# Kernel tuning notes

Measured on AMD Instinct MI355X. Metric: run time of the kernel, lower is better.

The kernel has to match this reference:

```python
import jax, jax.numpy as jnp
import numpy as np

DEPTH, FEAT, HID = 20, 2048, 1024
HALF = FEAT // 2
CLAMP = 2.0
TWO_OVER_PI = 0.6366197723675814  # FrEIA's 0.636619772


def setup_inputs() -> dict:
    key = jax.random.key(0)
    ks = jax.random.split(key, 9)
    x = jax.random.normal(ks[0], (4096, FEAT), dtype=jnp.float32)
    # FrEIA PermuteRandom: numpy permutation seeded with layer index k
    perms = jnp.asarray(
        np.stack([np.random.RandomState(k).permutation(FEAT) for k in range(DEPTH)]),
        dtype=jnp.int32,
    )
    def w(k, shape):  # module reinits all params as 0.01*randn
        return 0.01 * jax.random.normal(k, shape, dtype=jnp.float32)
    return {
        "x": x, "perms": perms,
        "s1_w1": w(ks[1], (DEPTH, HALF, HID)), "s1_b1": w(ks[2], (DEPTH, HID)),
        "s1_w2": w(ks[3], (DEPTH, HID, FEAT)), "s1_b2": w(ks[4], (DEPTH, FEAT)),
        "s2_w1": w(ks[5], (DEPTH, HALF, HID)), "s2_b1": w(ks[6], (DEPTH, HID)),
        "s2_w2": w(ks[7], (DEPTH, HID, FEAT)), "s2_b2": w(ks[8], (DEPTH, FEAT)),
    }


def _subnet(x, w1, b1, w2, b2):
    h = x @ w1 + b1
    h = jnp.where(h >= 0, h, 0.01 * h)  # LeakyReLU(negative_slope=0.01)
    return h @ w2 + b2


def reference(x, perms, s1_w1, s1_b1, s1_w2, s1_b2, s2_w1, s2_b1, s2_w2, s2_b2):
    def body(carry, xs):
        z, jac = carry
        perm, w1a, b1a, w1b, b1b, w2a, b2a, w2b, b2b = xs
        z = z[:, perm]                       # PermuteRandom
        x1, x2 = z[:, :HALF], z[:, HALF:]    # GLOW coupling split
        r2 = _subnet(x2, w2a, b2a, w2b, b2b)  # [B, FEAT] -> (s2, t2)
        e2 = CLAMP * TWO_OVER_PI * jnp.arctan(r2[:, :HALF] / CLAMP)
        y1 = jnp.exp(e2) * x1 + r2[:, HALF:]
        r1 = _subnet(y1, w1a, b1a, w1b, b1b)  # (s1, t1)
        e1 = CLAMP * TWO_OVER_PI * jnp.arctan(r1[:, :HALF] / CLAMP)
        y2 = jnp.exp(e1) * x2 + r1[:, HALF:]
        jac = jac + e1.sum(-1) + e2.sum(-1)  # log|det J| per sample
        return (jnp.concatenate([y1, y2], axis=-1), jac), None

    jac0 = jnp.zeros(x.shape[0], dtype=x.dtype)
    (z, jac), _ = jax.lax.scan(
        body, (x, jac0),
        (perms, s1_w1, s1_b1, s1_w2, s1_b2, s2_w1, s2_b1, s2_w2, s2_b2),
    )
    return z, jac
```

## Files before the change

kernel.cpp:

```cpp
#include <hip/hip_runtime.h>
#include <stdint.h>

#define DEPTH 20
#define FEAT  2048
#define HALF  1024
#define HID   1024
#define MROWS 4096

typedef __bf16 bf16x8 __attribute__((ext_vector_type(8)));
typedef float  f32x4  __attribute__((ext_vector_type(4)));
typedef unsigned int u32x4 __attribute__((ext_vector_type(4)));

__device__ __forceinline__ unsigned short f2bf(float f) {
  union { float f; unsigned int u; } v; v.f = f;
  unsigned int u = v.u + 0x7fffu + ((v.u >> 16) & 1u);
  return (unsigned short)(u >> 16);
}

__device__ __forceinline__ void async_cp16(unsigned short* lds, const unsigned short* g) {
  __builtin_amdgcn_global_load_lds(
      (const __attribute__((address_space(1))) void*)g,
      (__attribute__((address_space(3))) void*)lds, 16, 0, 0);
}

__device__ __forceinline__ bf16x8 lds_ld8(const unsigned short* p) {
  return __builtin_bit_cast(bf16x8, *(const u32x4*)p);
}

__global__ void wcvt_k(const float* __restrict__ s2w1, const float* __restrict__ s2w2,
                       const float* __restrict__ s1w1, const float* __restrict__ s1w2,
                       unsigned short* __restrict__ w2a, unsigned short* __restrict__ w2b,
                       unsigned short* __restrict__ w1a, unsigned short* __restrict__ w1b) {
  const int zid = blockIdx.z;
  const int d = zid >> 2, which = zid & 3;
  const float* src; unsigned short* dst; int N, pp;
  switch (which) {
    case 0:  src = s2w1 + (size_t)d * HALF * HID;  dst = w2a + (size_t)d * HALF * HID; N = 1024; pp = 0; break;
    case 1:  src = s2w2 + (size_t)d * HID * FEAT;  dst = w2b + (size_t)d * FEAT * HID; N = 2048; pp = 1; break;
    case 2:  src = s1w1 + (size_t)d * HALF * HID;  dst = w1a + (size_t)d * HALF * HID; N = 1024; pp = 0; break;
    default: src = s1w2 + (size_t)d * HID * FEAT;  dst = w1b + (size_t)d * FEAT * HID; N = 2048; pp = 1; break;
  }
  int nb = blockIdx.x * 32;
  if (nb >= N) return;
  int kb = blockIdx.y * 32;
  __shared__ float t[32][33];
  int tx = threadIdx.x, ty = threadIdx.y;
#pragma unroll
  for (int s = 0; s < 4; ++s)
    t[ty + 8*s][tx] = src[(size_t)(kb + ty + 8*s) * N + nb + tx];
  __syncthreads();
  int pbase = pp ? (nb < 1024 ? 2*nb : 2*(nb - 1024) + 32) : nb;
#pragma unroll
  for (int s = 0; s < 4; ++s) {
    int nl = ty + 8*s;
    dst[(size_t)(pbase + nl) * 1024 + kb + tx] = f2bf(t[tx][nl]);
  }
}

__device__ __forceinline__ int porig(int p) {
  int g = p >> 6, o = p & 63;
  return (o < 32) ? (g*32 + o) : (1024 + g*32 + (o - 32));
}

__global__ void bias_k(const float* __restrict__ s2b1, const float* __restrict__ s2b2,
                       const float* __restrict__ s1b1, const float* __restrict__ s1b2,
                       float* __restrict__ b2a, float* __restrict__ b2b,
                       float* __restrict__ b1a, float* __restrict__ b1b) {
  int i = blockIdx.x * 256 + threadIdx.x;
  if (i >= DEPTH * 6144) return;
  int d = i / 6144, j = i - d * 6144;
  if (j < 1024)      b2a[d*1024 + j] = s2b1[(size_t)d*HID + j];
  else if (j < 3072) { int p = j - 1024; b2b[d*2048 + p] = s2b2[(size_t)d*FEAT + porig(p)]; }
  else if (j < 4096) b1a[d*1024 + j - 3072] = s1b1[(size_t)d*HID + j - 3072];
  else               { int p = j - 4096; b1b[d*2048 + p] = s1b2[(size_t)d*FEAT + porig(p)]; }
}

__global__ void permute_k(const float* __restrict__ z, const int* __restrict__ perm,
                          float* __restrict__ x1f, float* __restrict__ x2f,
                          unsigned short* __restrict__ x2b) {
  int c = blockIdx.x * 256 + threadIdx.x;
  int row0 = blockIdx.y * 8;
  int pc = perm[c];
#pragma unroll
  for (int r = 0; r < 8; ++r) {
    int row = row0 + r;
    float v = z[row * FEAT + pc];
    if (c < HALF) {
      x1f[row * HALF + c] = v;
    } else {
      x2f[row * HALF + c - HALF] = v;
      x2b[row * HALF + c - HALF] = f2bf(v);
    }
  }
}

template<int EPI>
__launch_bounds__(256)
__global__ void gemm_k(const unsigned short* __restrict__ A,
                       const unsigned short* __restrict__ Bt,
                       const float* __restrict__ bias,
                       const float* __restrict__ xin,
                       float* __restrict__ yout,
                       unsigned short* __restrict__ ybf,
                       float* __restrict__ jac,
                       unsigned short* __restrict__ hout) {
  __shared__ unsigned short As[64 * 64];
  __shared__ unsigned short Bs[128 * 64];
  const int tid  = threadIdx.x;
  const int wave = tid >> 6, lane = tid & 63;
  const int quad = lane >> 4, l15 = lane & 15;
  const int wy = wave >> 1, wx = wave & 1;
  const int bm = blockIdx.y * 64;
  const int bn = blockIdx.x * 128;
  const int K = 1024;

  f32x4 acc[2][4];
#pragma unroll
  for (int i = 0; i < 2; ++i)
#pragma unroll
    for (int j = 0; j < 4; ++j)
#pragma unroll
      for (int r = 0; r < 4; ++r) acc[i][j][r] = 0.0f;

  const int gbase = wave * 64 + lane;

  for (int kt = 0; kt < 16; ++kt) {
    const int k0 = kt * 64;
#pragma unroll
    for (int i = 0; i < 2; ++i) {
      int g  = i * 256 + gbase;
      int r  = g >> 3, kg = (g & 7) ^ (r & 7);
      async_cp16(&As[(i * 256 + wave * 64) * 8], A + (size_t)(bm + r) * K + k0 + kg * 8);
    }
#pragma unroll
    for (int i = 0; i < 4; ++i) {
      int g  = i * 256 + gbase;
      int r  = g >> 3, kg = (g & 7) ^ (r & 7);
      async_cp16(&Bs[(i * 256 + wave * 64) * 8], Bt + (size_t)(bn + r) * K + k0 + kg * 8);
    }
    asm volatile("s_waitcnt vmcnt(0)" ::: "memory");
    __syncthreads();

#pragma unroll
    for (int kk = 0; kk < 2; ++kk) {
      bf16x8 af[2], bf[4];
#pragma unroll
      for (int i = 0; i < 2; ++i) {
        int ar = wy * 32 + i * 16 + l15;
        af[i] = lds_ld8(&As[ar * 64 + (((kk * 4 + quad) ^ (ar & 7))) * 8]);
      }
#pragma unroll
      for (int j = 0; j < 4; ++j) {
        int br = wx * 64 + j * 16 + l15;
        bf[j] = lds_ld8(&Bs[br * 64 + (((kk * 4 + quad) ^ (br & 7))) * 8]);
      }
#pragma unroll
      for (int i = 0; i < 2; ++i)
#pragma unroll
        for (int j = 0; j < 4; ++j)
          acc[i][j] = __builtin_amdgcn_mfma_f32_16x16x32_bf16(af[i], bf[j], acc[i][j], 0, 0, 0);
    }
    __syncthreads();
  }

  if (EPI == 0) {
    const int ldo = gridDim.x * 128;
#pragma unroll
    for (int j = 0; j < 4; ++j) {
      int col = bn + wx * 64 + j * 16 + l15;
      float bj = bias[col];
#pragma unroll
      for (int i = 0; i < 2; ++i) {
#pragma unroll
        for (int r = 0; r < 4; ++r) {
          int row = bm + wy * 32 + i * 16 + quad * 4 + r;
          float v = acc[i][j][r] + bj;
          v = v >= 0.0f ? v : 0.01f * v;
          hout[(size_t)row * ldo + col] = f2bf(v);
        }
      }
    }
  } else {
    const int g = (bn >> 6) + wx;
#pragma unroll
    for (int i = 0; i < 2; ++i) {
      float esum[4] = {0.0f, 0.0f, 0.0f, 0.0f};
#pragma unroll
      for (int j = 0; j < 2; ++j) {
        int pe = bn + wx * 64 + j * 16 + l15;
        float be = bias[pe];
        float ba = bias[pe + 32];
        int xcol = g * 32 + j * 16 + l15;
#pragma unroll
        for (int r = 0; r < 4; ++r) {
          int row = bm + wy * 32 + i * 16 + quad * 4 + r;
          float re = acc[i][j][r] + be;
          float ra = acc[i][j + 2][r] + ba;
          float e  = 1.2732395447351628f * atanf(0.5f * re);
          float y  = __expf(e) * xin[(size_t)row * HALF + xcol] + ra;
          yout[(size_t)row * FEAT + xcol] = y;
          if (ybf) ybf[(size_t)row * HALF + xcol] = f2bf(y);
          esum[r] += e;
        }
      }
#pragma unroll
      for (int r = 0; r < 4; ++r) {
        float v = esum[r];
        v += __shfl_xor(v, 1);
        v += __shfl_xor(v, 2);
        v += __shfl_xor(v, 4);
        v += __shfl_xor(v, 8);
        if (l15 == 0) {
          int row = bm + wy * 32 + i * 16 + quad * 4 + r;
          atomicAdd(&jac[row], v);
        }
      }
    }
  }
}

__global__ void jcopy_k(const float* __restrict__ jac, float* __restrict__ out) {
  int i = blockIdx.x * 256 + threadIdx.x;
  if (i < 4096) out[i] = jac[i];
}

extern "C" void kernel_launch(void* const* d_in, const int* in_sizes, int n_in,
                              void* d_out, int out_size, void* d_ws, size_t ws_size,
                              hipStream_t stream) {
  const float* x     = (const float*)d_in[0];
  const int*   perms = (const int*)d_in[1];
  const float* s1w1  = (const float*)d_in[2];
  const float* s1b1  = (const float*)d_in[3];
  const float* s1w2  = (const float*)d_in[4];
  const float* s1b2  = (const float*)d_in[5];
  const float* s2w1  = (const float*)d_in[6];
  const float* s2b1  = (const float*)d_in[7];
  const float* s2w2  = (const float*)d_in[8];
  const float* s2b2  = (const float*)d_in[9];
  float* out = (float*)d_out;

  size_t off = 0;
  char* base = (char*)d_ws;
  auto alloc = [&](size_t bytes) {
    void* r = base + off;
    off += (bytes + 255) & ~(size_t)255;
    return r;
  };
  float*          x1f = (float*)alloc((size_t)MROWS * HALF * 4);
  float*          x2f = (float*)alloc((size_t)MROWS * HALF * 4);
  unsigned short* x2b = (unsigned short*)alloc((size_t)MROWS * HALF * 2);
  unsigned short* y1b = (unsigned short*)alloc((size_t)MROWS * HALF * 2);
  unsigned short* hb  = (unsigned short*)alloc((size_t)MROWS * HID * 2);
  float*          zbuf= (float*)alloc((size_t)MROWS * FEAT * 4);
  unsigned short* w2a = (unsigned short*)alloc((size_t)DEPTH * HALF * HID * 2);
  unsigned short* w2b = (unsigned short*)alloc((size_t)DEPTH * FEAT * HID * 2);
  unsigned short* w1a = (unsigned short*)alloc((size_t)DEPTH * HALF * HID * 2);
  unsigned short* w1b = (unsigned short*)alloc((size_t)DEPTH * FEAT * HID * 2);
  float* b2a = (float*)alloc((size_t)DEPTH * 1024 * 4);
  float* b2b = (float*)alloc((size_t)DEPTH * 2048 * 4);
  float* b1a = (float*)alloc((size_t)DEPTH * 1024 * 4);
  float* b1b = (float*)alloc((size_t)DEPTH * 2048 * 4);
  float* jac = (float*)alloc(4096 * 4);

  hipMemsetAsync(jac, 0, 4096 * 4, stream);

  wcvt_k<<<dim3(64, 32, 4 * DEPTH), dim3(32, 8), 0, stream>>>(
      s2w1, s2w2, s1w1, s1w2, w2a, w2b, w1a, w1b);
  bias_k<<<(DEPTH * 6144 + 255) / 256, 256, 0, stream>>>(
      s2b1, s2b2, s1b1, s1b2, b2a, b2b, b1a, b1b);

  for (int d = 0; d < DEPTH; ++d) {
    const float* zsrc = (d == 0) ? x : zbuf;
    permute_k<<<dim3(8, 512), 256, 0, stream>>>(zsrc, perms + (size_t)d * FEAT, x1f, x2f, x2b);

    unsigned short* W2a = w2a + (size_t)d * HALF * HID;
    unsigned short* W2b = w2b + (size_t)d * FEAT * HID;
    unsigned short* W1a = w1a + (size_t)d * HALF * HID;
    unsigned short* W1b = w1b + (size_t)d * FEAT * HID;
    float* B2a = b2a + (size_t)d * 1024;
    float* B2b = b2b + (size_t)d * 2048;
    float* B1a = b1a + (size_t)d * 1024;
    float* B1b = b1b + (size_t)d * 2048;

    float* zdst = (d == DEPTH - 1) ? out : zbuf;
    gemm_k<0><<<dim3(8, 64), 256, 0, stream>>>(x2b, W2a, B2a, nullptr, nullptr, nullptr, nullptr, hb);
    gemm_k<1><<<dim3(16, 64), 256, 0, stream>>>(hb, W2b, B2b, x1f, zdst, y1b, jac, nullptr);
    gemm_k<0><<<dim3(8, 64), 256, 0, stream>>>(y1b, W1a, B1a, nullptr, nullptr, nullptr, nullptr, hb);
    gemm_k<1><<<dim3(16, 64), 256, 0, stream>>>(hb, W1b, B1b, x2f, zdst + HALF, nullptr, jac, nullptr);
  }
  jcopy_k<<<16, 256, 0, stream>>>(jac, out + (size_t)MROWS * FEAT);
}
```

Baseline: 3.503 ms.

## Gather x1 inside coupling epilogue and deepen K tile for hidden GEMMs

The permute kernel now only materializes the x2 half. The first coupling GEMM's epilogue reads x1 directly from the previous z through the permutation indices, using ping-pong z buffers so the source is not overwritten while it is read. This removes the x1f write and read traffic per layer, at the cost of an uncoalesced gather in the epilogue. Separately, the N=1024 GEMMs use a 128-wide K tile, which doubles LDS use per block and halves the number of barrier iterations.

```diff
diff --git a/kernel.cpp b/kernel.cpp
--- a/kernel.cpp
+++ b/kernel.cpp
@@ -76,36 +76,34 @@
 }
 
 __global__ void permute_k(const float* __restrict__ z, const int* __restrict__ perm,
-                          float* __restrict__ x1f, float* __restrict__ x2f,
-                          unsigned short* __restrict__ x2b) {
+                          float* __restrict__ x2f, unsigned short* __restrict__ x2b) {
   int c = blockIdx.x * 256 + threadIdx.x;
   int row0 = blockIdx.y * 8;
-  int pc = perm[c];
+  int pc = perm[HALF + c];
 #pragma unroll
   for (int r = 0; r < 8; ++r) {
     int row = row0 + r;
     float v = z[row * FEAT + pc];
-    if (c < HALF) {
-      x1f[row * HALF + c] = v;
-    } else {
-      x2f[row * HALF + c - HALF] = v;
-      x2b[row * HALF + c - HALF] = f2bf(v);
-    }
-  }
-}
-
-template<int EPI>
+    x2f[row * HALF + c] = v;
+    x2b[row * HALF + c] = f2bf(v);
+  }
+}
+
+template<int EPI, int BK>
 __launch_bounds__(256)
 __global__ void gemm_k(const unsigned short* __restrict__ A,
                        const unsigned short* __restrict__ Bt,
                        const float* __restrict__ bias,
                        const float* __restrict__ xin,
+                       const int* __restrict__ permg,
                        float* __restrict__ yout,
                        unsigned short* __restrict__ ybf,
                        float* __restrict__ jac,
                        unsigned short* __restrict__ hout) {
-  __shared__ unsigned short As[64 * 64];
-  __shared__ unsigned short Bs[128 * 64];
+  constexpr int CH = BK / 8;
+  constexpr int CM = CH - 1;
+  __shared__ unsigned short As[64 * BK];
+  __shared__ unsigned short Bs[128 * BK];
   const int tid  = threadIdx.x;
   const int wave = tid >> 6, lane = tid & 63;
   const int quad = lane >> 4, l15 = lane & 15;
@@ -124,35 +122,35 @@
 
   const int gbase = wave * 64 + lane;
 
-  for (int kt = 0; kt < 16; ++kt) {
-    const int k0 = kt * 64;
-#pragma unroll
-    for (int i = 0; i < 2; ++i) {
+  for (int kt = 0; kt < 1024 / BK; ++kt) {
+    const int k0 = kt * BK;
+#pragma unroll
+    for (int i = 0; i < CH / 4; ++i) {
       int g  = i * 256 + gbase;
-      int r  = g >> 3, kg = (g & 7) ^ (r & 7);
+      int r  = g / CH, kg = (g & CM) ^ (r & CM);
       async_cp16(&As[(i * 256 + wave * 64) * 8], A + (size_t)(bm + r) * K + k0 + kg * 8);
     }
 #pragma unroll
-    for (int i = 0; i < 4; ++i) {
+    for (int i = 0; i < CH / 2; ++i) {
       int g  = i * 256 + gbase;
-      int r  = g >> 3, kg = (g & 7) ^ (r & 7);
+      int r  = g / CH, kg = (g & CM) ^ (r & CM);
       async_cp16(&Bs[(i * 256 + wave * 64) * 8], Bt + (size_t)(bn + r) * K + k0 + kg * 8);
     }
     asm volatile("s_waitcnt vmcnt(0)" ::: "memory");
     __syncthreads();
 
 #pragma unroll
-    for (int kk = 0; kk < 2; ++kk) {
+    for (int kk = 0; kk < BK / 32; ++kk) {
       bf16x8 af[2], bf[4];
 #pragma unroll
       for (int i = 0; i < 2; ++i) {
         int ar = wy * 32 + i * 16 + l15;
-        af[i] = lds_ld8(&As[ar * 64 + (((kk * 4 + quad) ^ (ar & 7))) * 8]);
+        af[i] = lds_ld8(&As[ar * BK + ((kk * 4 + quad) ^ (ar & CM)) * 8]);
       }
 #pragma unroll
       for (int j = 0; j < 4; ++j) {
         int br = wx * 64 + j * 16 + l15;
-        bf[j] = lds_ld8(&Bs[br * 64 + (((kk * 4 + quad) ^ (br & 7))) * 8]);
+        bf[j] = lds_ld8(&Bs[br * BK + ((kk * 4 + quad) ^ (br & CM)) * 8]);
       }
 #pragma unroll
       for (int i = 0; i < 2; ++i)
@@ -182,24 +180,31 @@
     }
   } else {
     const int g = (bn >> 6) + wx;
+    float be[2], ba[2];
+    int xcol[2], pc[2];
+#pragma unroll
+    for (int j = 0; j < 2; ++j) {
+      int pe = bn + wx * 64 + j * 16 + l15;
+      be[j] = bias[pe];
+      ba[j] = bias[pe + 32];
+      xcol[j] = g * 32 + j * 16 + l15;
+      pc[j] = permg ? permg[xcol[j]] : xcol[j];
+    }
+    const size_t xstride = permg ? FEAT : HALF;
 #pragma unroll
     for (int i = 0; i < 2; ++i) {
       float esum[4] = {0.0f, 0.0f, 0.0f, 0.0f};
 #pragma unroll
       for (int j = 0; j < 2; ++j) {
-        int pe = bn + wx * 64 + j * 16 + l15;
-        float be = bias[pe];
-        float ba = bias[pe + 32];
-        int xcol = g * 32 + j * 16 + l15;
 #pragma unroll
         for (int r = 0; r < 4; ++r) {
           int row = bm + wy * 32 + i * 16 + quad * 4 + r;
-          float re = acc[i][j][r] + be;
-          float ra = acc[i][j + 2][r] + ba;
+          float re = acc[i][j][r] + be[j];
+          float ra = acc[i][j + 2][r] + ba[j];
           float e  = 1.2732395447351628f * atanf(0.5f * re);
-          float y  = __expf(e) * xin[(size_t)row * HALF + xcol] + ra;
-          yout[(size_t)row * FEAT + xcol] = y;
-          if (ybf) ybf[(size_t)row * HALF + xcol] = f2bf(y);
+          float y  = __expf(e) * xin[(size_t)row * xstride + pc[j]] + ra;
+          yout[(size_t)row * FEAT + xcol[j]] = y;
+          if (ybf) ybf[(size_t)row * HALF + xcol[j]] = f2bf(y);
           esum[r] += e;
         }
       }
@@ -246,12 +251,12 @@
     off += (bytes + 255) & ~(size_t)255;
     return r;
   };
-  float*          x1f = (float*)alloc((size_t)MROWS * HALF * 4);
   float*          x2f = (float*)alloc((size_t)MROWS * HALF * 4);
   unsigned short* x2b = (unsigned short*)alloc((size_t)MROWS * HALF * 2);
   unsigned short* y1b = (unsigned short*)alloc((size_t)MROWS * HALF * 2);
   unsigned short* hb  = (unsigned short*)alloc((size_t)MROWS * HID * 2);
-  float*          zbuf= (float*)alloc((size_t)MROWS * FEAT * 4);
+  float*          zA  = (float*)alloc((size_t)MROWS * FEAT * 4);
+  float*          zB  = (float*)alloc((size_t)MROWS * FEAT * 4);
   unsigned short* w2a = (unsigned short*)alloc((size_t)DEPTH * HALF * HID * 2);
   unsigned short* w2b = (unsigned short*)alloc((size_t)DEPTH * FEAT * HID * 2);
   unsigned short* w1a = (unsigned short*)alloc((size_t)DEPTH * HALF * HID * 2);
@@ -269,9 +274,13 @@
   bias_k<<<(DEPTH * 6144 + 255) / 256, 256, 0, stream>>>(
       s2b1, s2b2, s1b1, s1b2, b2a, b2b, b1a, b1b);
 
+  float* zping[2] = { zA, zB };
   for (int d = 0; d < DEPTH; ++d) {
-    const float* zsrc = (d == 0) ? x : zbuf;
-    permute_k<<<dim3(8, 512), 256, 0, stream>>>(zsrc, perms + (size_t)d * FEAT, x1f, x2f, x2b);
+    const float* zsrc = (d == 0) ? x : zping[(d + 1) & 1];
+    float* zdst = (d == DEPTH - 1) ? out : zping[d & 1];
+    const int* permd = perms + (size_t)d * FEAT;
+
+    permute_k<<<dim3(4, 512), 256, 0, stream>>>(zsrc, permd, x2f, x2b);
 
     unsigned short* W2a = w2a + (size_t)d * HALF * HID;
     unsigned short* W2b = w2b + (size_t)d * FEAT * HID;
@@ -282,11 +291,14 @@
     float* B1a = b1a + (size_t)d * 1024;
     float* B1b = b1b + (size_t)d * 2048;
 
-    float* zdst = (d == DEPTH - 1) ? out : zbuf;
-    gemm_k<0><<<dim3(8, 64), 256, 0, stream>>>(x2b, W2a, B2a, nullptr, nullptr, nullptr, nullptr, hb);
-    gemm_k<1><<<dim3(16, 64), 256, 0, stream>>>(hb, W2b, B2b, x1f, zdst, y1b, jac, nullptr);
-    gemm_k<0><<<dim3(8, 64), 256, 0, stream>>>(y1b, W1a, B1a, nullptr, nullptr, nullptr, nullptr, hb);
-    gemm_k<1><<<dim3(16, 64), 256, 0, stream>>>(hb, W1b, B1b, x2f, zdst + HALF, nullptr, jac, nullptr);
+    gemm_k<0, 128><<<dim3(8, 64), 256, 0, stream>>>(
+        x2b, W2a, B2a, nullptr, nullptr, nullptr, nullptr, nullptr, hb);
+    gemm_k<1, 64><<<dim3(16, 64), 256, 0, stream>>>(
+        hb, W2b, B2b, zsrc, permd, zdst, y1b, jac, nullptr);
+    gemm_k<0, 128><<<dim3(8, 64), 256, 0, stream>>>(
+        y1b, W1a, B1a, nullptr, nullptr, nullptr, nullptr, nullptr, hb);
+    gemm_k<1, 64><<<dim3(16, 64), 256, 0, stream>>>(
+        hb, W1b, B1b, x2f, nullptr, zdst + HALF, nullptr, jac, nullptr);
   }
   jcopy_k<<<16, 256, 0, stream>>>(jac, out + (size_t)MROWS * FEAT);
 }
```

Result: slower. 3.740 ms (+6.8%).
